# Kernel tuning notes

Measured on AMD Instinct MI355X. Metric: run time of the kernel, lower is better.

Reference implementation:

```python
import jax, jax.numpy as jnp
import numpy as np

B, S, D, H = 4, 2048, 1024, 16
HD = D // H          # head_dim = 64; per-head scale = sqrt(HD) as in source
FF = 4096
EPS = 1e-5


def _layernorm(x, g, b):
    m = jnp.mean(x, axis=-1, keepdims=True)
    v = jnp.mean(jnp.square(x - m), axis=-1, keepdims=True)
    return (x - m) * jax.lax.rsqrt(v + EPS) * g + b


def setup_inputs() -> dict:
    key = jax.random.key(0)
    ks = jax.random.split(key, 10)
    std = 0.02
    return {
        "x": jax.random.normal(ks[0], (B, S, D), jnp.float32),
        "wq": jax.random.normal(ks[1], (H, D, HD), jnp.float32) * std,
        "bq": jnp.zeros((H, HD), jnp.float32),
        "wk": jax.random.normal(ks[2], (H, D, HD), jnp.float32) * std,
        "bk": jnp.zeros((H, HD), jnp.float32),
        "wv": jax.random.normal(ks[3], (H, D, HD), jnp.float32) * std,
        "bv": jnp.zeros((H, HD), jnp.float32),
        "wo": jax.random.normal(ks[4], (D, D), jnp.float32) * std,
        "bo": jnp.zeros((D,), jnp.float32),
        "w1": jax.random.normal(ks[5], (D, FF), jnp.float32) * std,
        "b1": jnp.zeros((FF,), jnp.float32),
        "w2": jax.random.normal(ks[6], (FF, D), jnp.float32) * std,
        "b2": jnp.zeros((D,), jnp.float32),
        "g1": jnp.ones((D,), jnp.float32),
        "beta1": jnp.zeros((D,), jnp.float32),
        "g2": jnp.ones((D,), jnp.float32),
        "beta2": jnp.zeros((D,), jnp.float32),
    }


def reference(x, wq, bq, wk, bk, wv, bv, wo, bo, w1, b1, w2, b2, g1, beta1, g2, beta2):
    # Per-head Q/K/V projections (stacked over heads) -> [B,H,S,HD]
    q = jnp.einsum('bsd,hdf->bhsf', x, wq) + bq[None, :, None, :]
    k = jnp.einsum('bsd,hdf->bhsf', x, wk) + bk[None, :, None, :]
    v = jnp.einsum('bsd,hdf->bhsf', x, wv) + bv[None, :, None, :]

    scale = jnp.sqrt(jnp.asarray(HD, jnp.float32))
    att = jnp.einsum('bhqf,bhkf->bhqk', q, k) / scale  # [B,H,S,S]
    causal = jnp.tril(jnp.ones((S, S), dtype=bool))
    att = jnp.where(causal[None, None], att, -jnp.inf)
    p = jax.nn.softmax(att, axis=-1)
    o = jnp.einsum('bhqk,bhkf->bhqf', p, v)            # [B,H,S,HD]
    o = o.transpose(0, 2, 1, 3).reshape(B, S, D)       # concat heads
    attn_out = o @ wo + bo

    h = _layernorm(x + attn_out, g1, beta1)            # post-LN, dropout=0 (eval)
    ff = jax.nn.gelu(h @ w1 + b1, approximate=False) @ w2 + b2
    return _layernorm(h + ff, g2, beta2)
```

## Files before the change

### kernel.cpp

```cpp
#include <hip/hip_runtime.h>
#include <hip/hip_bf16.h>
#include <math.h>

typedef __bf16 bf16x8 __attribute__((ext_vector_type(8)));
typedef float floatx4 __attribute__((ext_vector_type(4)));
typedef unsigned short ushort8 __attribute__((ext_vector_type(8)));
typedef unsigned short ushort4v __attribute__((ext_vector_type(4)));

__device__ __forceinline__ unsigned short f2bs(float f){
  union { float f; unsigned u; } v; v.f = f;
  unsigned r = v.u + 0x7fffu + ((v.u >> 16) & 1u);
  return (unsigned short)(r >> 16);
}
__device__ __forceinline__ float bs2f(unsigned short s){
  union { unsigned u; float f; } v; v.u = ((unsigned)s) << 16; return v.f;
}
__device__ __forceinline__ unsigned pk2(float a, float b){
  union { __hip_bfloat162 h; unsigned u; } cv;
  cv.h = __float22bfloat162_rn(make_float2(a, b));
  return cv.u;
}
__device__ __forceinline__ void gl_lds16(const void* g, void* l){
  __builtin_amdgcn_global_load_lds(
      (const __attribute__((address_space(1))) void*)g,
      (__attribute__((address_space(3))) void*)l,
      16, 0, 0);
}

__global__ __launch_bounds__(256) void cvt_x(const float* __restrict__ x,
                                             unsigned short* __restrict__ o){
  const int i = (blockIdx.x*256 + threadIdx.x)*4;
  const float4 v = *(const float4*)(x + i);
  ushort4v u = { f2bs(v.x), f2bs(v.y), f2bs(v.z), f2bs(v.w) };
  *(ushort4v*)(o + i) = u;
}

__global__ __launch_bounds__(256) void transpose_pack(const float* __restrict__ src,
                                                      unsigned short* __restrict__ dst,
                                                      int R, int C){
  __shared__ float tile[32][65];
  const int r0 = blockIdx.y*32, c0 = blockIdx.x*64;
  const int t = threadIdx.x;
  {
    const int r = t >> 3, cc = (t & 7)*8;
    const float* p = src + (size_t)(r0+r)*C + c0 + cc;
    const float4 v0 = *(const float4*)p;
    const float4 v1 = *(const float4*)(p+4);
    tile[r][cc+0]=v0.x; tile[r][cc+1]=v0.y; tile[r][cc+2]=v0.z; tile[r][cc+3]=v0.w;
    tile[r][cc+4]=v1.x; tile[r][cc+5]=v1.y; tile[r][cc+6]=v1.z; tile[r][cc+7]=v1.w;
  }
  __syncthreads();
  const int f = t >> 2, rr = (t & 3)*8;
  ushort8 u;
  #pragma unroll
  for (int j=0;j<8;j++) u[j] = f2bs(tile[rr+j][f]);
  *(ushort8*)(dst + (size_t)(c0+f)*R + r0 + rr) = u;
}

__global__ __launch_bounds__(256) void pack_qkv(const float* __restrict__ wq,
                                                const float* __restrict__ wk,
                                                const float* __restrict__ wv,
                                                const float* __restrict__ bq,
                                                const float* __restrict__ bk,
                                                const float* __restrict__ bv,
                                                unsigned short* __restrict__ Wt,
                                                float* __restrict__ Bc){
  __shared__ float tile[32][65];
  const int dt = blockIdx.x, h = blockIdx.y, sel = blockIdx.z;
  const float* src = (sel==0 ? wq : (sel==1 ? wk : wv)) + (size_t)h*65536;
  const int t = threadIdx.x, d0 = dt*32;
  {
    const int r = t >> 3, cc = (t & 7)*8;
    const float* p = src + (size_t)(d0+r)*64 + cc;
    const float4 v0 = *(const float4*)p;
    const float4 v1 = *(const float4*)(p+4);
    tile[r][cc+0]=v0.x; tile[r][cc+1]=v0.y; tile[r][cc+2]=v0.z; tile[r][cc+3]=v0.w;
    tile[r][cc+4]=v1.x; tile[r][cc+5]=v1.y; tile[r][cc+6]=v1.z; tile[r][cc+7]=v1.w;
  }
  __syncthreads();
  const int f = t >> 2, rr = (t & 3)*8;
  ushort8 u;
  #pragma unroll
  for (int j=0;j<8;j++) u[j] = f2bs(tile[rr+j][f]);
  const size_t n = (size_t)sel*1024 + h*64 + f;
  *(ushort8*)(Wt + n*1024 + d0 + rr) = u;
  if (dt==0 && t<64){
    const float* bs = (sel==0 ? bq : (sel==1 ? bk : bv)) + h*64;
    Bc[sel*1024 + h*64 + t] = bs[t];
  }
}

template<int MODE>
__global__ __launch_bounds__(256, 4)
void gemm_tn(const unsigned short* __restrict__ A,
             const unsigned short* __restrict__ Bt,
             const float* __restrict__ bias,
             void* __restrict__ out0,
             void* __restrict__ out1,
             void* __restrict__ out2,
             int K, int OW, int klen){
  __shared__ __align__(16) unsigned short As[128*32];
  __shared__ __align__(16) unsigned short Bs[128*32];
  const int tid = threadIdx.x;
  const int wave = tid >> 6, lane = tid & 63;
  const int quad = lane >> 4, l15 = lane & 15;
  const int lin = blockIdx.x;
  const int n0 = (lin & 63) << 7;
  const int m0 = (lin >> 6) << 7;
  const int kz = blockIdx.z;
  const int kbase = kz * klen;
  const int wr = (wave >> 1) << 6, wc = (wave & 1) << 6;

  floatx4 acc[4][4];
  #pragma unroll
  for (int i=0;i<4;i++)
    #pragma unroll
    for (int j=0;j<4;j++) acc[i][j] = (floatx4)0.0f;

  const unsigned short* gA[2];
  const unsigned short* gB[2];
  int lofs[2];
  #pragma unroll
  for (int r2=0;r2<2;r2++){
    const int slot = r2*256 + tid;
    const int rp = slot >> 3, rem = slot & 7;
    const int row = rp*2 + (rem >> 2);
    const int kc = (rem & 3) ^ (rp & 3);
    gA[r2] = A  + (size_t)(m0 + row)*K + kbase + kc*8;
    gB[r2] = Bt + (size_t)(n0 + row)*K + kbase + kc*8;
    lofs[r2] = slot*8;
  }
  int aofs[4], bofs[4];
  #pragma unroll
  for (int t=0;t<4;t++){
    const int ra = wr + t*16 + l15;
    aofs[t] = (ra>>1)*64 + (ra&1)*32 + ((quad ^ ((ra>>1)&3))<<3);
    const int rb = wc + t*16 + l15;
    bofs[t] = (rb>>1)*64 + (rb&1)*32 + ((quad ^ ((rb>>1)&3))<<3);
  }

  for (int k0 = 0; k0 < klen; k0 += 32){
    gl_lds16(gA[0] + k0, As + lofs[0]);
    gl_lds16(gA[1] + k0, As + lofs[1]);
    gl_lds16(gB[0] + k0, Bs + lofs[0]);
    gl_lds16(gB[1] + k0, Bs + lofs[1]);
    __syncthreads();
    bf16x8 af[4];
    #pragma unroll
    for (int t=0;t<4;t++) af[t] = *(const bf16x8*)(&As[aofs[t]]);
    #pragma unroll
    for (int j=0;j<4;j++){
      const bf16x8 bv = *(const bf16x8*)(&Bs[bofs[j]]);
      #pragma unroll
      for (int i=0;i<4;i++)
        acc[i][j] = __builtin_amdgcn_mfma_f32_16x16x32_bf16(af[i], bv, acc[i][j], 0,0,0);
    }
    __syncthreads();
  }

  #pragma unroll
  for (int i=0;i<4;i++){
    const int row0 = m0 + wr + i*16 + quad*4;
    float4 b4 = make_float4(0.f,0.f,0.f,0.f);
    if (MODE != 4 || kz == 0) b4 = *(const float4*)(bias + row0);
    #pragma unroll
    for (int j=0;j<4;j++){
      const int tok = n0 + wc + j*16 + l15;
      float v0 = acc[i][j][0] + b4.x;
      float v1 = acc[i][j][1] + b4.y;
      float v2 = acc[i][j][2] + b4.z;
      float v3 = acc[i][j][3] + b4.w;
      if (MODE == 1){
        float4 o4; o4.x=v0; o4.y=v1; o4.z=v2; o4.w=v3;
        *(float4*)((float*)out0 + (size_t)tok*OW + row0) = o4;
      } else if (MODE == 2){
        float vv[4] = {v0,v1,v2,v3};
        #pragma unroll
        for (int r=0;r<4;r++){
          const float v = vv[r];
          const float u = 0.7978845608f*v*(1.0f + 0.044715f*v*v);
          const float e = __builtin_amdgcn_exp2f(u * 2.885390082f);
          vv[r] = 0.5f*v*(1.0f + (1.0f - 2.0f/(1.0f + e)));
        }
        uint2 pkd = make_uint2(pk2(vv[0], vv[1]), pk2(vv[2], vv[3]));
        *(uint2*)((unsigned short*)out0 + (size_t)tok*4096 + row0) = pkd;
      } else if (MODE == 4){
        uint2 pkd = make_uint2(pk2(v0, v1), pk2(v2, v3));
        unsigned short* o = (unsigned short*)(kz ? out1 : out0);
        *(uint2*)(o + (size_t)tok*1024 + row0) = pkd;
      } else {
        if (row0 < 1024){
          const float s = 0.18033688011112042f;
          uint2 pkd = make_uint2(pk2(v0*s, v1*s), pk2(v2*s, v3*s));
          *(uint2*)((unsigned short*)out0 + (size_t)tok*1024 + row0) = pkd;
        } else if (row0 < 2048){
          uint2 pkd = make_uint2(pk2(v0, v1), pk2(v2, v3));
          *(uint2*)((unsigned short*)out1 + (size_t)tok*1024 + (row0-1024)) = pkd;
        } else {
          uint2 pkd = make_uint2(pk2(v0, v1), pk2(v2, v3));
          *(uint2*)((unsigned short*)out2 + (size_t)tok*1024 + (row0-2048)) = pkd;
        }
      }
    }
  }
}

__global__ __launch_bounds__(256) void vtrans(const unsigned short* __restrict__ Vtok,
                                              unsigned short* __restrict__ Vt){
  __shared__ unsigned short tile[64][65];
  const int st = blockIdx.x, bh = blockIdx.y;
  const int b = bh >> 4, h = bh & 15;
  const int t = threadIdx.x;
  {
    const int r = t >> 2, cc = (t & 3) * 16;
    const unsigned short* src = Vtok + (size_t)((b<<11) + (st<<6) + r)*1024 + (h<<6) + cc;
    ushort8 u0 = *(const ushort8*)src;
    ushort8 u1 = *(const ushort8*)(src + 8);
    #pragma unroll
    for (int j=0;j<8;j++){ tile[r][cc+j] = u0[j]; tile[r][cc+8+j] = u1[j]; }
  }
  __syncthreads();
  const int f = t >> 2, ss = (t & 3) * 16;
  ushort8 w0, w1;
  #pragma unroll
  for (int j=0;j<8;j++){ w0[j] = tile[ss+j][f]; w1[j] = tile[ss+8+j][f]; }
  unsigned short* dst = Vt + (size_t)bh*64*2048 + (size_t)f*2048 + (st<<6) + ss;
  *(ushort8*)dst = w0;
  *(ushort8*)(dst + 8) = w1;
}

__global__ __launch_bounds__(256, 3) void attn(const unsigned short* __restrict__ Q,
                                               const unsigned short* __restrict__ Kg,
                                               const unsigned short* __restrict__ Vt,
                                               unsigned short* __restrict__ O){
  __shared__ __align__(16) unsigned short Ks[64*64];
  __shared__ __align__(16) unsigned short Vs[64*64];
  __shared__ __align__(16) unsigned short PT[4][2][16*68];

  const int lin = blockIdx.x;
  const int bh = lin & 63;
  const int qt_lo = lin >> 6;
  const int qt_hi = 31 - qt_lo;
  const int b = bh >> 4, h = bh & 15;
  const int tid = threadIdx.x, wave = tid >> 6, lane = tid & 63;
  const int quad = lane >> 4, l15 = lane & 15;
  const float FM = 12.0f;

  const size_t qbase = (size_t)((b<<11) + (wave<<4) + l15)*1024 + (h<<6);
  bf16x8 qf_hi[2], qf_lo[2];
  qf_hi[0] = *(const bf16x8*)(Q + qbase + (size_t)(qt_hi<<6)*1024 + quad*8);
  qf_hi[1] = *(const bf16x8*)(Q + qbase + (size_t)(qt_hi<<6)*1024 + 32 + quad*8);
  qf_lo[0] = *(const bf16x8*)(Q + qbase + (size_t)(qt_lo<<6)*1024 + quad*8);
  qf_lo[1] = *(const bf16x8*)(Q + qbase + (size_t)(qt_lo<<6)*1024 + 32 + quad*8);

  floatx4 oa_hi[4], oa_lo[4];
  #pragma unroll
  for (int i=0;i<4;i++){ oa_hi[i] = (floatx4)0.0f; oa_lo[i] = (floatx4)0.0f; }
  float li_hi = 0.0f, li_lo = 0.0f;

  const unsigned short* Kbh = Kg + ((size_t)(b<<11))*1024 + (h<<6);
  const unsigned short* Vbh = Vt + (size_t)bh*64*2048;
  unsigned short* Pw0 = &PT[wave][0][0];
  unsigned short* Pw1 = &PT[wave][1][0];

  const int slot0 = wave*128 + lane;
  const int krow0 = slot0 >> 3, kc0 = (slot0 & 7) ^ (krow0 & 7);
  const int slot1 = slot0 + 64;
  const int krow1 = slot1 >> 3, kc1 = (slot1 & 7) ^ (krow1 & 7);

  auto softmax_P = [&](floatx4* sa, float& li, unsigned short* Pbuf, bool diag){
    if (diag){
      const int qrow = (wave<<4) + l15;
      #pragma unroll
      for (int tj=0;tj<4;tj++)
        #pragma unroll
        for (int r=0;r<4;r++)
          if (tj*16 + quad*4 + r > qrow) sa[tj][r] = -1e30f;
    }
    float rs = 0.0f;
    #pragma unroll
    for (int tj=0;tj<4;tj++)
      #pragma unroll
      for (int r=0;r<4;r++){
        const float p = __builtin_amdgcn_exp2f(sa[tj][r] - FM);
        sa[tj][r] = p;
        rs += p;
      }
    li += rs;
    #pragma unroll
    for (int tj=0;tj<4;tj++){
      uint2 pkd = make_uint2(pk2(sa[tj][0], sa[tj][1]), pk2(sa[tj][2], sa[tj][3]));
      *(uint2*)(Pbuf + l15*68 + tj*16 + quad*4) = pkd;
    }
  };

  for (int kt = 0; kt <= qt_hi; ++kt){
    gl_lds16(Kbh + (size_t)((kt<<6) + krow0)*1024 + kc0*8, Ks + wave*1024);
    gl_lds16(Kbh + (size_t)((kt<<6) + krow1)*1024 + kc1*8, Ks + wave*1024 + 512);
    gl_lds16(Vbh + (size_t)krow0*2048 + (kt<<6) + kc0*8, Vs + wave*1024);
    gl_lds16(Vbh + (size_t)krow1*2048 + (kt<<6) + kc1*8, Vs + wave*1024 + 512);
    __syncthreads();

    if (kt <= qt_lo){
      floatx4 sh[4], sl[4];
      #pragma unroll
      for (int tj=0;tj<4;tj++){
        sh[tj] = (floatx4)0.0f; sl[tj] = (floatx4)0.0f;
        #pragma unroll
        for (int ks=0;ks<2;ks++){
          const int n = tj*16 + l15;
          const int c = (ks*4 + quad) ^ (n & 7);
          const bf16x8 kf = *(const bf16x8*)(Ks + n*64 + c*8);
          sh[tj] = __builtin_amdgcn_mfma_f32_16x16x32_bf16(kf, qf_hi[ks], sh[tj], 0,0,0);
          sl[tj] = __builtin_amdgcn_mfma_f32_16x16x32_bf16(kf, qf_lo[ks], sl[tj], 0,0,0);
        }
      }
      softmax_P(sh, li_hi, Pw0, false);
      softmax_P(sl, li_lo, Pw1, kt == qt_lo);
      #pragma unroll
      for (int ks2=0;ks2<2;ks2++){
        const bf16x8 pfh = *(const bf16x8*)(Pw0 + l15*68 + ks2*32 + quad*8);
        const bf16x8 pfl = *(const bf16x8*)(Pw1 + l15*68 + ks2*32 + quad*8);
        #pragma unroll
        for (int tn=0;tn<4;tn++){
          const int n2 = tn*16 + l15;
          const int c = (ks2*4 + quad) ^ (n2 & 7);
          const bf16x8 vf = *(const bf16x8*)(Vs + n2*64 + c*8);
          oa_hi[tn] = __builtin_amdgcn_mfma_f32_16x16x32_bf16(vf, pfh, oa_hi[tn], 0,0,0);
          oa_lo[tn] = __builtin_amdgcn_mfma_f32_16x16x32_bf16(vf, pfl, oa_lo[tn], 0,0,0);
        }
      }
    } else {
      floatx4 sh[4];
      #pragma unroll
      for (int tj=0;tj<4;tj++){
        sh[tj] = (floatx4)0.0f;
        #pragma unroll
        for (int ks=0;ks<2;ks++){
          const int n = tj*16 + l15;
          const int c = (ks*4 + quad) ^ (n & 7);
          const bf16x8 kf = *(const bf16x8*)(Ks + n*64 + c*8);
          sh[tj] = __builtin_amdgcn_mfma_f32_16x16x32_bf16(kf, qf_hi[ks], sh[tj], 0,0,0);
        }
      }
      softmax_P(sh, li_hi, Pw0, kt == qt_hi);
      #pragma unroll
      for (int ks2=0;ks2<2;ks2++){
        const bf16x8 pfh = *(const bf16x8*)(Pw0 + l15*68 + ks2*32 + quad*8);
        #pragma unroll
        for (int tn=0;tn<4;tn++){
          const int n2 = tn*16 + l15;
          const int c = (ks2*4 + quad) ^ (n2 & 7);
          const bf16x8 vf = *(const bf16x8*)(Vs + n2*64 + c*8);
          oa_hi[tn] = __builtin_amdgcn_mfma_f32_16x16x32_bf16(vf, pfh, oa_hi[tn], 0,0,0);
        }
      }
    }
    __syncthreads();
  }

  li_hi += __shfl_xor(li_hi, 16, 64);
  li_hi += __shfl_xor(li_hi, 32, 64);
  li_lo += __shfl_xor(li_lo, 16, 64);
  li_lo += __shfl_xor(li_lo, 32, 64);
  {
    const float inv = 1.0f / li_hi;
    unsigned short* Orow = O + (size_t)((b<<11) + (qt_hi<<6) + (wave<<4) + l15)*1024 + (h<<6);
    #pragma unroll
    for (int tn=0;tn<4;tn++){
      uint2 pkd = make_uint2(pk2(oa_hi[tn][0]*inv, oa_hi[tn][1]*inv),
                             pk2(oa_hi[tn][2]*inv, oa_hi[tn][3]*inv));
      *(uint2*)(Orow + tn*16 + quad*4) = pkd;
    }
  }
  {
    const float inv = 1.0f / li_lo;
    unsigned short* Orow = O + (size_t)((b<<11) + (qt_lo<<6) + (wave<<4) + l15)*1024 + (h<<6);
    #pragma unroll
    for (int tn=0;tn<4;tn++){
      uint2 pkd = make_uint2(pk2(oa_lo[tn][0]*inv, oa_lo[tn][1]*inv),
                             pk2(oa_lo[tn][2]*inv, oa_lo[tn][3]*inv));
      *(uint2*)(Orow + tn*16 + quad*4) = pkd;
    }
  }
}

__global__ __launch_bounds__(256) void ln_res(const float* __restrict__ a,
                                              const float* __restrict__ bsrc,
                                              const float* __restrict__ g,
                                              const float* __restrict__ be,
                                              float* __restrict__ of,
                                              unsigned short* __restrict__ ob){
  __shared__ float red1[4], red2[4];
  const int row = blockIdx.x, t = threadIdx.x;
  const int wave = t >> 6, lane = t & 63;
  const float4 va = *(const float4*)(a + (size_t)row*1024 + t*4);
  const float4 vb = *(const float4*)(bsrc + (size_t)row*1024 + t*4);
  float xs[4] = {va.x+vb.x, va.y+vb.y, va.z+vb.z, va.w+vb.w};
  float s = xs[0]+xs[1]+xs[2]+xs[3];
  #pragma unroll
  for (int d=1; d<64; d<<=1) s += __shfl_xor(s, d, 64);
  if (lane==0) red1[wave] = s;
  __syncthreads();
  const float mean = (red1[0]+red1[1]+red1[2]+red1[3]) * (1.0f/1024.0f);
  float vsum = 0.0f;
  #pragma unroll
  for (int i=0;i<4;i++){ const float d = xs[i]-mean; vsum += d*d; }
  #pragma unroll
  for (int d=1; d<64; d<<=1) vsum += __shfl_xor(vsum, d, 64);
  if (lane==0) red2[wave] = vsum;
  __syncthreads();
  const float var = (red2[0]+red2[1]+red2[2]+red2[3]) * (1.0f/1024.0f);
  const float rs = rsqrtf(var + 1e-5f);
  const float4 gg = *(const float4*)(g + t*4);
  const float4 bb = *(const float4*)(be + t*4);
  float y[4];
  y[0] = (xs[0]-mean)*rs*gg.x + bb.x;
  y[1] = (xs[1]-mean)*rs*gg.y + bb.y;
  y[2] = (xs[2]-mean)*rs*gg.z + bb.z;
  y[3] = (xs[3]-mean)*rs*gg.w + bb.w;
  if (of){
    float4 o4; o4.x=y[0]; o4.y=y[1]; o4.z=y[2]; o4.w=y[3];
    *(float4*)(of + (size_t)row*1024 + t*4) = o4;
  }
  if (ob){
    ushort4v u = { f2bs(y[0]), f2bs(y[1]), f2bs(y[2]), f2bs(y[3]) };
    *(ushort4v*)(ob + (size_t)row*1024 + t*4) = u;
  }
}

__global__ __launch_bounds__(256) void ln_res2(const float* __restrict__ a,
                                               const unsigned short* __restrict__ p0,
                                               const unsigned short* __restrict__ p1,
                                               const float* __restrict__ g,
                                               const float* __restrict__ be,
                                               float* __restrict__ of){
  __shared__ float red1[4], red2[4];
  const int row = blockIdx.x, t = threadIdx.x;
  const int wave = t >> 6, lane = t & 63;
  const float4 va = *(const float4*)(a + (size_t)row*1024 + t*4);
  const ushort4v u0 = *(const ushort4v*)(p0 + (size_t)row*1024 + t*4);
  const ushort4v u1 = *(const ushort4v*)(p1 + (size_t)row*1024 + t*4);
  float xs[4] = { va.x + bs2f(u0[0]) + bs2f(u1[0]),
                  va.y + bs2f(u0[1]) + bs2f(u1[1]),
                  va.z + bs2f(u0[2]) + bs2f(u1[2]),
                  va.w + bs2f(u0[3]) + bs2f(u1[3]) };
  float s = xs[0]+xs[1]+xs[2]+xs[3];
  #pragma unroll
  for (int d=1; d<64; d<<=1) s += __shfl_xor(s, d, 64);
  if (lane==0) red1[wave] = s;
  __syncthreads();
  const float mean = (red1[0]+red1[1]+red1[2]+red1[3]) * (1.0f/1024.0f);
  float vsum = 0.0f;
  #pragma unroll
  for (int i=0;i<4;i++){ const float d = xs[i]-mean; vsum += d*d; }
  #pragma unroll
  for (int d=1; d<64; d<<=1) vsum += __shfl_xor(vsum, d, 64);
  if (lane==0) red2[wave] = vsum;
  __syncthreads();
  const float var = (red2[0]+red2[1]+red2[2]+red2[3]) * (1.0f/1024.0f);
  const float rs = rsqrtf(var + 1e-5f);
  const float4 gg = *(const float4*)(g + t*4);
  const float4 bb = *(const float4*)(be + t*4);
  float4 o4;
  o4.x = (xs[0]-mean)*rs*gg.x + bb.x;
  o4.y = (xs[1]-mean)*rs*gg.y + bb.y;
  o4.z = (xs[2]-mean)*rs*gg.z + bb.z;
  o4.w = (xs[3]-mean)*rs*gg.w + bb.w;
  *(float4*)(of + (size_t)row*1024 + t*4) = o4;
}

extern "C" void kernel_launch(void* const* d_in, const int* in_sizes, int n_in,
                              void* d_out, int out_size, void* d_ws, size_t ws_size,
                              hipStream_t stream){
  (void)in_sizes; (void)n_in; (void)out_size; (void)ws_size;
  const float* x  = (const float*)d_in[0];
  const float* wq = (const float*)d_in[1];
  const float* bq = (const float*)d_in[2];
  const float* wk = (const float*)d_in[3];
  const float* bk = (const float*)d_in[4];
  const float* wv = (const float*)d_in[5];
  const float* bv = (const float*)d_in[6];
  const float* wo = (const float*)d_in[7];
  const float* bo = (const float*)d_in[8];
  const float* w1 = (const float*)d_in[9];
  const float* b1 = (const float*)d_in[10];
  const float* w2 = (const float*)d_in[11];
  const float* b2 = (const float*)d_in[12];
  const float* g1 = (const float*)d_in[13];
  const float* be1= (const float*)d_in[14];
  const float* g2 = (const float*)d_in[15];
  const float* be2= (const float*)d_in[16];
  float* out = (float*)d_out;

  char* ws = (char*)d_ws;
  size_t off = 0;
  auto take = [&](size_t bytes)->char*{
    char* p = ws + off; off += (bytes + 255) & ~(size_t)255; return p;
  };
  unsigned short* Xb  = (unsigned short*)take(8192UL*1024*2);
  unsigned short* Qb  = (unsigned short*)take(8192UL*1024*2);
  unsigned short* Kb  = (unsigned short*)take(8192UL*1024*2);
  unsigned short* Vtb = (unsigned short*)take(8192UL*1024*2);
  unsigned short* Ob  = (unsigned short*)take(8192UL*1024*2);
  unsigned short* Midb= Qb;
  unsigned short* Vtok= (unsigned short*)take(8192UL*1024*2);
  unsigned short* Wqkv= (unsigned short*)take(3072UL*1024*2);
  float*          Bqkv= (float*)take(3072UL*4);
  unsigned short* Wot = (unsigned short*)take(1024UL*1024*2);
  unsigned short* W1t = (unsigned short*)take(4096UL*1024*2);
  unsigned short* W2t = (unsigned short*)take(1024UL*4096*2);
  float*          C1  = (float*)take(8192UL*1024*4);
  unsigned short* F0  = (unsigned short*)C1;
  unsigned short* F1  = F0 + 8192UL*1024;
  float*          Hf  = (float*)take(8192UL*1024*4);
  unsigned short* Hb  = (unsigned short*)take(8192UL*1024*2);

  cvt_x<<<8192, 256, 0, stream>>>(x, Xb);
  pack_qkv<<<dim3(32,16,3), 256, 0, stream>>>(wq, wk, wv, bq, bk, bv, Wqkv, Bqkv);
  transpose_pack<<<dim3(16,32),  256, 0, stream>>>(wo, Wot, 1024, 1024);
  transpose_pack<<<dim3(64,32),  256, 0, stream>>>(w1, W1t, 1024, 4096);
  transpose_pack<<<dim3(16,128), 256, 0, stream>>>(w2, W2t, 4096, 1024);

  gemm_tn<3><<<24*64, 256, 0, stream>>>(Wqkv, Xb, Bqkv, Qb, Kb, Vtok, 1024, 0, 1024);
  vtrans<<<dim3(32,64), 256, 0, stream>>>(Vtok, Vtb);

  attn<<<1024, 256, 0, stream>>>(Qb, Kb, Vtb, Ob);

  gemm_tn<1><<<8*64, 256, 0, stream>>>(Wot, Ob, bo, C1, nullptr, nullptr, 1024, 1024, 1024);
  ln_res<<<8192, 256, 0, stream>>>(x, C1, g1, be1, Hf, Hb);

  gemm_tn<2><<<32*64, 256, 0, stream>>>(W1t, Hb, b1, Midb, nullptr, nullptr, 1024, 4096, 1024);
  gemm_tn<4><<<dim3(8*64,1,2), 256, 0, stream>>>(W2t, Midb, b2, F0, F1, nullptr, 4096, 1024, 2048);
  ln_res2<<<8192, 256, 0, stream>>>(Hf, F0, F1, g2, be2, out);
}
```

Before: 567.0 us.

## Add 256x256-tile 8-wave GEMM with pipelined LDS staging for QKV and FFN

Adds a new GEMM kernel that uses 256x256 output tiles with 512 threads. It double-buffers K slices in LDS through direct global-to-LDS loads, with XOR-swizzled layout, interleaved staging across four sub-phases and raised wave priority around the MFMA blocks. The QKV projection and both FFN GEMMs switch to it, which gives more operand reuse per loaded byte and overlaps loads with compute. The trade-off is far fewer blocks (384/512/256), higher register pressure from 32 accumulators per wave, and a large LDS footprint that limits occupancy.

Measured after the change: 560.1 us. Within noise of the previous version (-1.2%).

```diff
diff --git a/kernel.cpp b/kernel.cpp
--- a/kernel.cpp
+++ b/kernel.cpp
@@ -199,6 +199,172 @@
         } else {
           uint2 pkd = make_uint2(pk2(v0, v1), pk2(v2, v3));
           *(uint2*)((unsigned short*)out2 + (size_t)tok*1024 + (row0-2048)) = pkd;
+        }
+      }
+    }
+  }
+}
+
+#define NOOP ((void)0)
+#define VMCNT4 asm volatile("s_waitcnt vmcnt(4)" ::: "memory")
+#define VMCNT0 asm volatile("s_waitcnt vmcnt(0)" ::: "memory")
+#define TAILW { if (tg < NT-2) VMCNT4; else VMCNT0; }
+
+#define STAGE_A(T, H) { const int T_ = (T); if (T_ < NT){                     \
+    unsigned short* l_ = lds + (T_&1)*32768 + (H)*8192;                       \
+    const int ko_ = kbase + (T_<<6);                                          \
+    gl_lds16(srcA##H##_0 + ko_, l_ + ch0*8);                                  \
+    gl_lds16(srcA##H##_1 + ko_, l_ + ch1*8); } }
+#define STAGE_B(T, H) { const int T_ = (T); if (T_ < NT){                     \
+    unsigned short* l_ = lds + (T_&1)*32768 + 16384 + (H)*8192;               \
+    const int ko_ = kbase + (T_<<6);                                          \
+    gl_lds16(srcB##H##_0 + ko_, l_ + ch0*8);                                  \
+    gl_lds16(srcB##H##_1 + ko_, l_ + ch1*8); } }
+
+#define PHASE(D, MH, NH, STAGE_STMT, TAIL_STMT)                               \
+  {                                                                           \
+    const unsigned short* Ab_ = lds + (D)*32768 + (MH)*8192;                  \
+    const unsigned short* Bb_ = lds + (D)*32768 + 16384 + (NH)*8192;          \
+    bf16x8 af_[4][2], bf_[2][2];                                              \
+    _Pragma("unroll")                                                         \
+    for (int m_=0;m_<4;m_++)                                                  \
+      _Pragma("unroll")                                                       \
+      for (int k_=0;k_<2;k_++) af_[m_][k_] = *(const bf16x8*)(Ab_ + aoff[m_][k_]); \
+    _Pragma("unroll")                                                         \
+    for (int n_=0;n_<2;n_++)                                                  \
+      _Pragma("unroll")                                                       \
+      for (int k_=0;k_<2;k_++) bf_[n_][k_] = *(const bf16x8*)(Bb_ + boff[n_][k_]); \
+    STAGE_STMT;                                                               \
+    __builtin_amdgcn_s_barrier();                                             \
+    asm volatile("s_waitcnt lgkmcnt(0)" ::: "memory");                        \
+    __builtin_amdgcn_sched_barrier(0);                                        \
+    __builtin_amdgcn_s_setprio(1);                                            \
+    _Pragma("unroll")                                                         \
+    for (int k_=0;k_<2;k_++)                                                  \
+      _Pragma("unroll")                                                       \
+      for (int m_=0;m_<4;m_++)                                                \
+        _Pragma("unroll")                                                     \
+        for (int n_=0;n_<2;n_++)                                              \
+          acc[(MH)*4+m_][(NH)*2+n_] = __builtin_amdgcn_mfma_f32_16x16x32_bf16( \
+              af_[m_][k_], bf_[n_][k_], acc[(MH)*4+m_][(NH)*2+n_], 0,0,0);    \
+    __builtin_amdgcn_s_setprio(0);                                            \
+    TAIL_STMT;                                                                \
+    __builtin_amdgcn_s_barrier();                                             \
+  }
+
+template<int MODE>
+__global__ __launch_bounds__(512, 2)
+void gemm256(const unsigned short* __restrict__ A,
+             const unsigned short* __restrict__ Bt,
+             const float* __restrict__ bias,
+             void* __restrict__ out0,
+             void* __restrict__ out1,
+             void* __restrict__ out2,
+             int K, int klen){
+  __shared__ __align__(16) unsigned short lds[65536];
+  const int tid = threadIdx.x;
+  const int wave = tid >> 6, lane = tid & 63;
+  const int quad = lane >> 4, l15 = lane & 15;
+  const int wm = wave >> 2, wn = wave & 3;
+  const int lin = blockIdx.x;
+  const int n0 = (lin & 31) << 8;
+  const int m0 = (lin >> 5) << 8;
+  const int kz = blockIdx.z;
+  const int kbase = kz * klen;
+  const int NT = klen >> 6;
+
+  const int r0 = tid >> 3;
+  const int r1 = r0 + 64;
+  const int g0 = (tid & 7) ^ (r0 & 7);
+  const int ch0 = tid, ch1 = tid + 512;
+
+  const unsigned short* srcA0_0 = A  + (size_t)(m0 +       r0)*K + g0*8;
+  const unsigned short* srcA0_1 = A  + (size_t)(m0 +       r1)*K + g0*8;
+  const unsigned short* srcA1_0 = A  + (size_t)(m0 + 128 + r0)*K + g0*8;
+  const unsigned short* srcA1_1 = A  + (size_t)(m0 + 128 + r1)*K + g0*8;
+  const unsigned short* srcB0_0 = Bt + (size_t)(n0 +       r0)*K + g0*8;
+  const unsigned short* srcB0_1 = Bt + (size_t)(n0 +       r1)*K + g0*8;
+  const unsigned short* srcB1_0 = Bt + (size_t)(n0 + 128 + r0)*K + g0*8;
+  const unsigned short* srcB1_1 = Bt + (size_t)(n0 + 128 + r1)*K + g0*8;
+
+  const int xr = l15 & 7;
+  int aoff[4][2], boff[2][2];
+  #pragma unroll
+  for (int m=0;m<4;m++){
+    const int rh = wm*64 + m*16 + l15;
+    #pragma unroll
+    for (int k=0;k<2;k++)
+      aoff[m][k] = rh*64 + (((k*4 + quad) ^ xr) << 3);
+  }
+  #pragma unroll
+  for (int n=0;n<2;n++){
+    const int rb = wn*32 + n*16 + l15;
+    #pragma unroll
+    for (int k=0;k<2;k++)
+      boff[n][k] = rb*64 + (((k*4 + quad) ^ xr) << 3);
+  }
+
+  floatx4 acc[8][4];
+  #pragma unroll
+  for (int i=0;i<8;i++)
+    #pragma unroll
+    for (int j=0;j<4;j++) acc[i][j] = (floatx4)0.0f;
+
+  STAGE_B(0,0); STAGE_A(0,0); STAGE_A(0,1); STAGE_B(0,1);
+  STAGE_B(1,0); STAGE_A(1,0);
+  VMCNT4;
+  __builtin_amdgcn_s_barrier();
+
+  for (int tg = 0; tg < NT; ++tg){
+    const int d = tg & 1;
+    PHASE(d, 0, 0, STAGE_A(tg+1, 1), NOOP);
+    PHASE(d, 1, 0, STAGE_B(tg+1, 1), NOOP);
+    PHASE(d, 0, 1, STAGE_B(tg+2, 0), NOOP);
+    PHASE(d, 1, 1, STAGE_A(tg+2, 0), TAILW);
+  }
+
+  #pragma unroll
+  for (int mh=0; mh<2; mh++){
+    #pragma unroll
+    for (int m=0; m<4; m++){
+      const int row0 = m0 + mh*128 + wm*64 + m*16 + quad*4;
+      float4 b4 = make_float4(0.f,0.f,0.f,0.f);
+      if (MODE != 4 || kz == 0) b4 = *(const float4*)(bias + row0);
+      #pragma unroll
+      for (int nh=0; nh<2; nh++){
+        #pragma unroll
+        for (int n=0; n<2; n++){
+          const int tok = n0 + nh*128 + wn*32 + n*16 + l15;
+          const floatx4 a = acc[mh*4+m][nh*2+n];
+          float v0 = a[0]+b4.x, v1 = a[1]+b4.y, v2 = a[2]+b4.z, v3 = a[3]+b4.w;
+          if (MODE == 2){
+            float vv[4] = {v0,v1,v2,v3};
+            #pragma unroll
+            for (int r=0;r<4;r++){
+              const float v = vv[r];
+              const float u = 0.7978845608f*v*(1.0f + 0.044715f*v*v);
+              const float e = __builtin_amdgcn_exp2f(u * 2.885390082f);
+              vv[r] = 0.5f*v*(1.0f + (1.0f - 2.0f/(1.0f + e)));
+            }
+            uint2 pkd = make_uint2(pk2(vv[0], vv[1]), pk2(vv[2], vv[3]));
+            *(uint2*)((unsigned short*)out0 + (size_t)tok*4096 + row0) = pkd;
+          } else if (MODE == 4){
+            uint2 pkd = make_uint2(pk2(v0, v1), pk2(v2, v3));
+            unsigned short* o = (unsigned short*)(kz ? out1 : out0);
+            *(uint2*)(o + (size_t)tok*1024 + row0) = pkd;
+          } else {
+            if (row0 < 1024){
+              const float s = 0.18033688011112042f;
+              uint2 pkd = make_uint2(pk2(v0*s, v1*s), pk2(v2*s, v3*s));
+              *(uint2*)((unsigned short*)out0 + (size_t)tok*1024 + row0) = pkd;
+            } else if (row0 < 2048){
+              uint2 pkd = make_uint2(pk2(v0, v1), pk2(v2, v3));
+              *(uint2*)((unsigned short*)out1 + (size_t)tok*1024 + (row0-1024)) = pkd;
+            } else {
+              uint2 pkd = make_uint2(pk2(v0, v1), pk2(v2, v3));
+              *(uint2*)((unsigned short*)out2 + (size_t)tok*1024 + (row0-2048)) = pkd;
+            }
+          }
         }
       }
     }
@@ -522,7 +688,7 @@
   transpose_pack<<<dim3(64,32),  256, 0, stream>>>(w1, W1t, 1024, 4096);
   transpose_pack<<<dim3(16,128), 256, 0, stream>>>(w2, W2t, 4096, 1024);
 
-  gemm_tn<3><<<24*64, 256, 0, stream>>>(Wqkv, Xb, Bqkv, Qb, Kb, Vtok, 1024, 0, 1024);
+  gemm256<3><<<12*32, 512, 0, stream>>>(Wqkv, Xb, Bqkv, Qb, Kb, Vtok, 1024, 1024);
   vtrans<<<dim3(32,64), 256, 0, stream>>>(Vtok, Vtb);
 
   attn<<<1024, 256, 0, stream>>>(Qb, Kb, Vtb, Ob);
@@ -530,7 +696,7 @@
   gemm_tn<1><<<8*64, 256, 0, stream>>>(Wot, Ob, bo, C1, nullptr, nullptr, 1024, 1024, 1024);
   ln_res<<<8192, 256, 0, stream>>>(x, C1, g1, be1, Hf, Hb);
 
-  gemm_tn<2><<<32*64, 256, 0, stream>>>(W1t, Hb, b1, Midb, nullptr, nullptr, 1024, 4096, 1024);
-  gemm_tn<4><<<dim3(8*64,1,2), 256, 0, stream>>>(W2t, Midb, b2, F0, F1, nullptr, 4096, 1024, 2048);
+  gemm256<2><<<16*32, 512, 0, stream>>>(W1t, Hb, b1, Midb, nullptr, nullptr, 1024, 1024);
+  gemm256<4><<<dim3(4*32,1,2), 512, 0, stream>>>(W2t, Midb, b2, F0, F1, nullptr, 4096, 2048);
   ln_res2<<<8192, 256, 0, stream>>>(Hf, F0, F1, g2, be2, out);
 }
```
